# Kernel optimization log

Measured on AMD Instinct MI355X. Metric: run time of the kernel, lower is better.

The kernel has to match this reference:

```python
import jax, jax.numpy as jnp
import numpy as np

V = 16384      # total nodes
G = 32         # nodes per graph (512 graphs)
D = 256        # node embedding dim == hidden_size
N = 8          # heads
H = 32         # head size
I = 1024       # intermediate size
LN_EPS = 1e-12


def _layer_norm(x, g, b):
    mu = jnp.mean(x, axis=-1, keepdims=True)
    var = jnp.mean(jnp.square(x - mu), axis=-1, keepdims=True)
    return (x - mu) * jax.lax.rsqrt(var + LN_EPS) * g + b


def setup_inputs() -> dict:
    key = jax.random.key(0)
    ks = jax.random.split(key, 5)
    node_embeddings = jax.random.normal(ks[0], (V, D), jnp.float32)
    # fully-connected pairs within each graph of size G (sorted by source node)
    idx = np.arange(V, dtype=np.int32).reshape(-1, G)          # [num_graphs, G]
    src = np.repeat(idx, G, axis=1).reshape(-1)                # [P]
    dst = np.tile(idx, (1, G)).reshape(-1)                     # [P]
    in_graph_node_pairs = jnp.asarray(np.stack([src, dst], axis=-1))  # [P, 2]
    s = 0.02
    return {
        "node_embeddings": node_embeddings,
        "in_graph_node_pairs": in_graph_node_pairs,
        "W_qkv": jax.random.normal(ks[1], (D, 3 * N * H), jnp.float32) * s,
        "W_o": jax.random.normal(ks[2], (N * H, D), jnp.float32) * s,
        "ln1_g": jnp.ones((D,), jnp.float32),
        "ln1_b": jnp.zeros((D,), jnp.float32),
        "W_i": jax.random.normal(ks[3], (D, I), jnp.float32) * s,
        "W_out2": jax.random.normal(ks[4], (I, D), jnp.float32) * s,
        "ln2_g": jnp.ones((D,), jnp.float32),
        "ln2_b": jnp.zeros((D,), jnp.float32),
    }


def reference(node_embeddings, in_graph_node_pairs, W_qkv, W_o, ln1_g, ln1_b,
              W_i, W_out2, ln2_g, ln2_b):
    nV = node_embeddings.shape[0]
    src = in_graph_node_pairs[:, 0]
    dst = in_graph_node_pairs[:, 1]
    # QKV projection -> [V, N, 3H] -> split
    qkv = (node_embeddings @ W_qkv).reshape(nV, N, 3 * H)
    q, k, v = jnp.split(qkv, 3, axis=-1)                       # each [V, N, H]
    # per-pair scores [P, N]
    scores = jnp.einsum('phi,phi->ph', q[src], k[dst]) / jnp.sqrt(jnp.float32(H))
    # segment softmax over source node, all heads at once
    m = jax.ops.segment_max(scores, src, num_segments=nV)       # [V, N]
    e = jnp.exp(scores - m[src])
    denom = jax.ops.segment_sum(e, src, num_segments=nV)        # [V, N]
    w = e / denom[src]                                          # [P, N]
    # weighted value scatter-sum -> [V, N, H]
    wv = w[:, :, None] * v[dst]
    att = jax.ops.segment_sum(wv, src, num_segments=nV).reshape(nV, N * H)
    # output projection + residual + LN
    pre = _layer_norm(att @ W_o + node_embeddings, ln1_g, ln1_b)
    inter = jax.nn.gelu(pre @ W_i, approximate=False)
    out = _layer_norm(inter @ W_out2 + pre, ln2_g, ln2_b)
    return out
```

## Files before the change

### kernel.cpp

```cpp
#include <hip/hip_runtime.h>
#include <math.h>

#define V 16384
#define D 256
#define NH 256
#define THREE_NH 768
#define IDIM 1024
#define LN_EPS 1e-12f
#define SCL 0.17677669529663687f

typedef short s16x8 __attribute__((ext_vector_type(8)));
typedef float f32x4 __attribute__((ext_vector_type(4)));

__device__ inline unsigned short f2bf(float f) {
    unsigned u = __float_as_uint(f);
    u += 0x7fffu + ((u >> 16) & 1u);
    return (unsigned short)(u >> 16);
}
__device__ inline float bf2f(unsigned short s) {
    return __uint_as_float(((unsigned)s) << 16);
}

__device__ inline float fast_erf(float x) {
    float ax = fabsf(x);
    float t  = 1.f / fmaf(0.3275911f, ax, 1.f);
    float p  = fmaf(fmaf(fmaf(fmaf(1.061405429f, t, -1.453152027f), t,
                              1.421413741f), t, -0.284496736f), t, 0.254829592f);
    float e  = 1.f - p * t * __expf(-ax * ax);
    return copysignf(e, x);
}

__device__ inline void gl2lds16(const unsigned short* g, unsigned short* l) {
    __builtin_amdgcn_global_load_lds(
        (__attribute__((address_space(1))) void*)(g),
        (__attribute__((address_space(3))) void*)(l), 16, 0, 0);
}

template <int ROWS_T>
__device__ inline void stage(const unsigned short* __restrict__ src, size_t row0,
                             int ldk, int k0, unsigned short* lds, int wv, int lane) {
    constexpr int PER_WAVE = ROWS_T / 32;
    #pragma unroll
    for (int i = 0; i < PER_WAVE; ++i) {
        const int seg = wv * PER_WAVE + i;
        const int r = seg * 8 + (lane >> 3);
        const int c = (lane & 7) ^ (r & 7);
        gl2lds16(src + (row0 + (size_t)r) * ldk + k0 + c * 8, lds + seg * 512);
    }
}

__device__ inline s16x8 fragld(const unsigned short* lds, int row, int chunk) {
    return *(const s16x8*)&lds[row * 64 + ((chunk ^ (row & 7)) << 3)];
}

__global__ __launch_bounds__(256) void prep(const float* __restrict__ X,
                                            unsigned short* __restrict__ Xb,
                                            const float* __restrict__ Wqkv,
                                            const float* __restrict__ Wo,
                                            const float* __restrict__ Wi,
                                            const float* __restrict__ Wo2,
                                            unsigned short* __restrict__ WqkvT,
                                            unsigned short* __restrict__ WoT,
                                            unsigned short* __restrict__ WiT,
                                            unsigned short* __restrict__ Wo2T) {
    const int b = blockIdx.x, t = threadIdx.x;
    if (b >= 768) {
        int i = (b - 768) * 256 + t;
        float4 v = ((const float4*)X)[i];
        ushort4 o;
        o.x = f2bf(v.x); o.y = f2bf(v.y); o.z = f2bf(v.z); o.w = f2bf(v.w);
        ((ushort4*)Xb)[i] = o;
        return;
    }
    __shared__ float tile[32][33];
    const float* W; unsigned short* Wt; int K, N, bx, by;
    if (b < 192)      { W = Wqkv; Wt = WqkvT; K = 256;  N = 768;  bx = b & 7;          by = b >> 3; }
    else if (b < 256) { W = Wo;   Wt = WoT;   K = 256;  N = 256;  bx = (b - 192) & 7;  by = (b - 192) >> 3; }
    else if (b < 512) { W = Wi;   Wt = WiT;   K = 256;  N = 1024; bx = (b - 256) & 7;  by = (b - 256) >> 3; }
    else              { W = Wo2;  Wt = Wo2T;  K = 1024; N = 256;  bx = (b - 512) & 31; by = (b - 512) >> 5; }
    const int k0 = bx * 32, n0 = by * 32;
    #pragma unroll
    for (int p = 0; p < 4; ++p) {
        int idx = t + p * 256, r = idx >> 5, c = idx & 31;
        tile[r][c] = W[(size_t)(k0 + r) * N + n0 + c];
    }
    __syncthreads();
    #pragma unroll
    for (int p = 0; p < 4; ++p) {
        int idx = t + p * 256, r = idx >> 5, c = idx & 31;
        Wt[(size_t)(n0 + r) * K + k0 + c] = f2bf(tile[c][r]);
    }
}

template <int K, int N, int EPI>
__global__ __launch_bounds__(256) void gemm128(const unsigned short* __restrict__ A,
                                               const unsigned short* __restrict__ Bt,
                                               unsigned short* __restrict__ C) {
    __shared__ unsigned short As[128 * 64];
    __shared__ unsigned short Bs[128 * 64];
    constexpr int NCOL = N / 128;
    const int b = blockIdx.x;
    const int idx = b >> 3;
    const int r0 = ((b & 7) * 16 + idx / NCOL) * 128;
    const int c0 = (idx % NCOL) * 128;
    const int t = threadIdx.x;
    const int wv = t >> 6, lane = t & 63, q = lane >> 4, l16 = lane & 15;
    const int wr = (wv >> 1) * 64, wc = (wv & 1) * 64;
    f32x4 acc[4][4] = {};

    for (int k0 = 0; k0 < K; k0 += 64) {
        __syncthreads();
        stage<128>(A,  (size_t)r0, K, k0, As, wv, lane);
        stage<128>(Bt, (size_t)c0, K, k0, Bs, wv, lane);
        __builtin_amdgcn_s_waitcnt(0);
        __syncthreads();
        #pragma unroll
        for (int kk2 = 0; kk2 < 2; ++kk2) {
            s16x8 af[4], bfr[4];
            #pragma unroll
            for (int mf = 0; mf < 4; ++mf)
                af[mf] = fragld(As, wr + mf * 16 + l16, kk2 * 4 + q);
            #pragma unroll
            for (int nf = 0; nf < 4; ++nf)
                bfr[nf] = fragld(Bs, wc + nf * 16 + l16, kk2 * 4 + q);
            #pragma unroll
            for (int mf = 0; mf < 4; ++mf)
                #pragma unroll
                for (int nf = 0; nf < 4; ++nf)
                    acc[mf][nf] = __builtin_amdgcn_mfma_f32_16x16x32_bf16(af[mf], bfr[nf], acc[mf][nf], 0, 0, 0);
        }
    }

    #pragma unroll
    for (int mf = 0; mf < 4; ++mf)
        #pragma unroll
        for (int nf = 0; nf < 4; ++nf) {
            const int cg = c0 + wc + nf * 16 + l16;
            #pragma unroll
            for (int r = 0; r < 4; ++r) {
                const int rg = r0 + wr + mf * 16 + q * 4 + r;
                float v = acc[mf][nf][r];
                if (EPI == 1) v = 0.5f * v * (1.f + fast_erf(v * 0.70710678118654752f));
                C[(size_t)rg * N + cg] = f2bf(v);
            }
        }
}

template <int K, bool OUTF, bool RESBF>
__global__ __launch_bounds__(256) void gemm_ln(const unsigned short* __restrict__ A,
                                               const unsigned short* __restrict__ Bt,
                                               const void* __restrict__ resv,
                                               const float* __restrict__ gamma,
                                               const float* __restrict__ beta,
                                               float* __restrict__ outf,
                                               unsigned short* __restrict__ outb) {
    __shared__ unsigned short As[2][32 * 64];
    __shared__ unsigned short Bs[2][256 * 64];
    __shared__ float2 partial[4][32];
    __shared__ float2 stats[32];
    const int t = threadIdx.x, r0 = blockIdx.x * 32;
    const int wv = t >> 6, lane = t & 63, q = lane >> 4, l16 = lane & 15;
    const int wc = wv * 64;
    f32x4 acc[2][4] = {};

    for (int k0 = 0; k0 < K; k0 += 128) {
        __syncthreads();
        stage<32>(A, (size_t)r0, K, k0,      As[0], wv, lane);
        stage<32>(A, (size_t)r0, K, k0 + 64, As[1], wv, lane);
        stage<256>(Bt, 0, K, k0,      Bs[0], wv, lane);
        stage<256>(Bt, 0, K, k0 + 64, Bs[1], wv, lane);
        __builtin_amdgcn_s_waitcnt(0);
        __syncthreads();
        #pragma unroll
        for (int sub = 0; sub < 2; ++sub) {
            #pragma unroll
            for (int kk2 = 0; kk2 < 2; ++kk2) {
                s16x8 af[2], bfr[4];
                #pragma unroll
                for (int mf = 0; mf < 2; ++mf)
                    af[mf] = fragld(As[sub], mf * 16 + l16, kk2 * 4 + q);
                #pragma unroll
                for (int nf = 0; nf < 4; ++nf)
                    bfr[nf] = fragld(Bs[sub], wc + nf * 16 + l16, kk2 * 4 + q);
                #pragma unroll
                for (int mf = 0; mf < 2; ++mf)
                    #pragma unroll
                    for (int nf = 0; nf < 4; ++nf)
                        acc[mf][nf] = __builtin_amdgcn_mfma_f32_16x16x32_bf16(af[mf], bfr[nf], acc[mf][nf], 0, 0, 0);
            }
        }
    }

    #pragma unroll
    for (int mf = 0; mf < 2; ++mf)
        #pragma unroll
        for (int nf = 0; nf < 4; ++nf) {
            const int cg = wc + nf * 16 + l16;
            #pragma unroll
            for (int r = 0; r < 4; ++r) {
                const size_t idx = (size_t)(r0 + mf * 16 + q * 4 + r) * NH + cg;
                float rv;
                if (RESBF) rv = bf2f(((const unsigned short*)resv)[idx]);
                else       rv = ((const float*)resv)[idx];
                acc[mf][nf][r] += rv;
            }
        }

    #pragma unroll
    for (int mf = 0; mf < 2; ++mf) {
        float s[4] = {0.f, 0.f, 0.f, 0.f}, ss[4] = {0.f, 0.f, 0.f, 0.f};
        #pragma unroll
        for (int nf = 0; nf < 4; ++nf)
            #pragma unroll
            for (int r = 0; r < 4; ++r) {
                float v = acc[mf][nf][r];
                s[r] += v; ss[r] += v * v;
            }
        #pragma unroll
        for (int off = 1; off < 16; off <<= 1)
            #pragma unroll
            for (int r = 0; r < 4; ++r) {
                s[r]  += __shfl_xor(s[r],  off);
                ss[r] += __shfl_xor(ss[r], off);
            }
        if (l16 == 0)
            #pragma unroll
            for (int r = 0; r < 4; ++r)
                partial[wv][mf * 16 + q * 4 + r] = make_float2(s[r], ss[r]);
    }
    __syncthreads();
    if (t < 32) {
        float s = 0.f, ss = 0.f;
        #pragma unroll
        for (int w = 0; w < 4; ++w) { s += partial[w][t].x; ss += partial[w][t].y; }
        float mu  = s * (1.f / 256.f);
        float var = ss * (1.f / 256.f) - mu * mu;
        stats[t] = make_float2(mu, rsqrtf(var + LN_EPS));
    }
    __syncthreads();

    #pragma unroll
    for (int mf = 0; mf < 2; ++mf)
        #pragma unroll
        for (int nf = 0; nf < 4; ++nf) {
            const int cg = wc + nf * 16 + l16;
            const float g = gamma[cg], b = beta[cg];
            #pragma unroll
            for (int r = 0; r < 4; ++r) {
                const int rl = mf * 16 + q * 4 + r;
                const float2 st = stats[rl];
                float v = (acc[mf][nf][r] - st.x) * st.y * g + b;
                const size_t idx = (size_t)(r0 + rl) * NH + cg;
                if (OUTF) outf[idx] = v;
                else      outb[idx] = f2bf(v);
            }
        }
}

__global__ __launch_bounds__(256) void attln(const unsigned short* __restrict__ qkv,
                                             const unsigned short* __restrict__ WoT,
                                             const float* __restrict__ X,
                                             const float* __restrict__ gamma,
                                             const float* __restrict__ beta,
                                             unsigned short* __restrict__ preb) {
    __shared__ unsigned short smem[25216];
    unsigned short* Ks = smem;
    unsigned short* Vt = smem + 8192;
    unsigned short* Ps = smem + 16384;
    unsigned short* at = smem;
    unsigned short* Bs = smem + 8192;
    float2* partial = (float2*)(smem + 24576);
    float2* stats   = (float2*)(smem + 24576 + 512);

    const int g = blockIdx.x, t = threadIdx.x;
    const int wv = t >> 6, lane = t & 63, q = lane >> 4, l16 = lane & 15;
    const unsigned short* src = qkv + (size_t)g * 32 * THREE_NH;

    s16x8 qf[2][2];
    #pragma unroll
    for (int hh = 0; hh < 2; ++hh)
        #pragma unroll
        for (int mf = 0; mf < 2; ++mf)
            qf[hh][mf] = *(const s16x8*)&src[(size_t)(mf * 16 + l16) * THREE_NH +
                                             (wv * 2 + hh) * 96 + q * 8];

    s16x8 vld[4];
    int vh[4], vj[4], vdc[4];
    #pragma unroll
    for (int i = 0; i < 4; ++i) {
        int cid = i * 256 + t;
        vh[i] = cid >> 7; int rem = cid & 127; vj[i] = rem >> 2; vdc[i] = rem & 3;
        vld[i] = *(const s16x8*)&src[(size_t)vj[i] * THREE_NH + vh[i] * 96 + 64 + vdc[i] * 8];
    }

    #pragma unroll
    for (int i = 0; i < 4; ++i) {
        int ck = (wv * 4 + i) * 64 + lane;
        int h = ck >> 7, j = (ck >> 2) & 31, c = ck & 3;
        gl2lds16(src + (size_t)j * THREE_NH + h * 96 + 32 + c * 8, Ks + (wv * 4 + i) * 512);
    }

    #pragma unroll
    for (int i = 0; i < 4; ++i)
        #pragma unroll
        for (int e = 0; e < 8; ++e) {
            int d = vdc[i] * 8 + e;
            Vt[vh[i] * 1024 + d * 32 + ((((vj[i] >> 3) ^ ((d >> 2) & 3))) << 3) + (vj[i] & 7)] =
                (unsigned short)vld[i][e];
        }

    __builtin_amdgcn_s_waitcnt(0);
    __syncthreads();

    f32x4 sacc[2][2][2] = {};
    #pragma unroll
    for (int hh = 0; hh < 2; ++hh) {
        const int h = wv * 2 + hh;
        #pragma unroll
        for (int nf = 0; nf < 2; ++nf) {
            s16x8 kf = *(const s16x8*)&Ks[h * 1024 + (nf * 16 + l16) * 32 + q * 8];
            #pragma unroll
            for (int mf = 0; mf < 2; ++mf)
                sacc[hh][mf][nf] = __builtin_amdgcn_mfma_f32_16x16x32_bf16(
                    qf[hh][mf], kf, sacc[hh][mf][nf], 0, 0, 0);
        }
    }

    float inv[2][2][4];
    #pragma unroll
    for (int hh = 0; hh < 2; ++hh) {
        const int h = wv * 2 + hh;
        #pragma unroll
        for (int mf = 0; mf < 2; ++mf)
            #pragma unroll
            for (int r = 0; r < 4; ++r) {
                float a0 = sacc[hh][mf][0][r], a1 = sacc[hh][mf][1][r];
                float m = fmaxf(a0, a1);
                m = fmaxf(m, __shfl_xor(m, 1));
                m = fmaxf(m, __shfl_xor(m, 2));
                m = fmaxf(m, __shfl_xor(m, 4));
                m = fmaxf(m, __shfl_xor(m, 8));
                float e0 = __expf((a0 - m) * SCL);
                float e1 = __expf((a1 - m) * SCL);
                float sm = e0 + e1;
                sm += __shfl_xor(sm, 1);
                sm += __shfl_xor(sm, 2);
                sm += __shfl_xor(sm, 4);
                sm += __shfl_xor(sm, 8);
                inv[hh][mf][r] = 1.f / sm;
                const int row = mf * 16 + q * 4 + r;
                const int base = h * 1024 + row * 32 + (l16 & 7);
                Ps[base + ((((l16 >> 3) ^ q)) << 3)]       = f2bf(e0);
                Ps[base + ((((2 + (l16 >> 3)) ^ q)) << 3)] = f2bf(e1);
            }
    }

    f32x4 oacc[2][2][2] = {};
    #pragma unroll
    for (int hh = 0; hh < 2; ++hh) {
        const int h = wv * 2 + hh;
        const int sw = (l16 >> 2) & 3;
        s16x8 pa[2], vb[2];
        #pragma unroll
        for (int mf = 0; mf < 2; ++mf)
            pa[mf] = *(const s16x8*)&Ps[h * 1024 + (mf * 16 + l16) * 32 + ((q ^ sw) << 3)];
        #pragma unroll
        for (int nf = 0; nf < 2; ++nf)
            vb[nf] = *(const s16x8*)&Vt[h * 1024 + (nf * 16 + l16) * 32 + ((q ^ sw) << 3)];
        #pragma unroll
        for (int mf = 0; mf < 2; ++mf)
            #pragma unroll
            for (int nf = 0; nf < 2; ++nf)
                oacc[hh][mf][nf] = __builtin_amdgcn_mfma_f32_16x16x32_bf16(
                    pa[mf], vb[nf], oacc[hh][mf][nf], 0, 0, 0);
    }
    __syncthreads();

    #pragma unroll
    for (int hh = 0; hh < 2; ++hh)
        #pragma unroll
        for (int mf = 0; mf < 2; ++mf)
            #pragma unroll
            for (int nf = 0; nf < 2; ++nf)
                #pragma unroll
                for (int r = 0; r < 4; ++r) {
                    float val = oacc[hh][mf][nf][r] * inv[hh][mf][r];
                    const int i = mf * 16 + q * 4 + r;
                    const int col = (wv * 2 + hh) * 32 + nf * 16 + l16;
                    const int kb = col >> 6, c = (col >> 3) & 7;
                    at[kb * 2048 + i * 64 + ((c ^ (i & 7)) << 3) + (col & 7)] = f2bf(val);
                }

    const int wc = wv * 64;
    const int r0 = g * 32;
    f32x4 acc[2][4] = {};

    for (int k0 = 0; k0 < 256; k0 += 64) {
        __syncthreads();
        stage<256>(WoT, 0, 256, k0, Bs, wv, lane);
        __builtin_amdgcn_s_waitcnt(0);
        __syncthreads();
        const unsigned short* atk = at + (k0 >> 6) * 2048;
        #pragma unroll
        for (int kk2 = 0; kk2 < 2; ++kk2) {
            s16x8 af[2], bfr[4];
            #pragma unroll
            for (int mf = 0; mf < 2; ++mf)
                af[mf] = fragld(atk, mf * 16 + l16, kk2 * 4 + q);
            #pragma unroll
            for (int nf = 0; nf < 4; ++nf)
                bfr[nf] = fragld(Bs, wc + nf * 16 + l16, kk2 * 4 + q);
            #pragma unroll
            for (int mf = 0; mf < 2; ++mf)
                #pragma unroll
                for (int nf = 0; nf < 4; ++nf)
                    acc[mf][nf] = __builtin_amdgcn_mfma_f32_16x16x32_bf16(af[mf], bfr[nf], acc[mf][nf], 0, 0, 0);
        }
    }

    #pragma unroll
    for (int mf = 0; mf < 2; ++mf)
        #pragma unroll
        for (int nf = 0; nf < 4; ++nf) {
            const int cg = wc + nf * 16 + l16;
            #pragma unroll
            for (int r = 0; r < 4; ++r)
                acc[mf][nf][r] += X[(size_t)(r0 + mf * 16 + q * 4 + r) * NH + cg];
        }

    #pragma unroll
    for (int mf = 0; mf < 2; ++mf) {
        float sp[4] = {0.f, 0.f, 0.f, 0.f}, ssp[4] = {0.f, 0.f, 0.f, 0.f};
        #pragma unroll
        for (int nf = 0; nf < 4; ++nf)
            #pragma unroll
            for (int r = 0; r < 4; ++r) {
                float v = acc[mf][nf][r];
                sp[r] += v; ssp[r] += v * v;
            }
        #pragma unroll
        for (int off = 1; off < 16; off <<= 1)
            #pragma unroll
            for (int r = 0; r < 4; ++r) {
                sp[r]  += __shfl_xor(sp[r],  off);
                ssp[r] += __shfl_xor(ssp[r], off);
            }
        if (l16 == 0)
            #pragma unroll
            for (int r = 0; r < 4; ++r)
                partial[wv * 32 + mf * 16 + q * 4 + r] = make_float2(sp[r], ssp[r]);
    }
    __syncthreads();
    if (t < 32) {
        float sv = 0.f, ssv = 0.f;
        #pragma unroll
        for (int w = 0; w < 4; ++w) { sv += partial[w * 32 + t].x; ssv += partial[w * 32 + t].y; }
        float mu  = sv * (1.f / 256.f);
        float var = ssv * (1.f / 256.f) - mu * mu;
        stats[t] = make_float2(mu, rsqrtf(var + LN_EPS));
    }
    __syncthreads();

    #pragma unroll
    for (int mf = 0; mf < 2; ++mf)
        #pragma unroll
        for (int nf = 0; nf < 4; ++nf) {
            const int cg = wc + nf * 16 + l16;
            const float gm = gamma[cg], bt = beta[cg];
            #pragma unroll
            for (int r = 0; r < 4; ++r) {
                const int rl = mf * 16 + q * 4 + r;
                const float2 st = stats[rl];
                float v = (acc[mf][nf][r] - st.x) * st.y * gm + bt;
                preb[(size_t)(r0 + rl) * NH + cg] = f2bf(v);
            }
        }
}

extern "C" void kernel_launch(void* const* d_in, const int* in_sizes, int n_in,
                              void* d_out, int out_size, void* d_ws, size_t ws_size,
                              hipStream_t stream) {
    const float* X      = (const float*)d_in[0];
    const float* W_qkv  = (const float*)d_in[2];
    const float* W_o    = (const float*)d_in[3];
    const float* ln1_g  = (const float*)d_in[4];
    const float* ln1_b  = (const float*)d_in[5];
    const float* W_i    = (const float*)d_in[6];
    const float* W_out2 = (const float*)d_in[7];
    const float* ln2_g  = (const float*)d_in[8];
    const float* ln2_b  = (const float*)d_in[9];
    float* out = (float*)d_out;

    char* ws = (char*)d_ws;
    unsigned short* Xbf   = (unsigned short*)(ws);
    unsigned short* qkvb  = (unsigned short*)(ws + 8388608);
    unsigned short* preb  = (unsigned short*)(ws + 58720256);
    unsigned short* WqkvT = (unsigned short*)(ws + 67108864);
    unsigned short* WoT   = (unsigned short*)(ws + 67502080);
    unsigned short* WiT   = (unsigned short*)(ws + 67633152);
    unsigned short* Wo2T  = (unsigned short*)(ws + 68157440);
    unsigned short* interb = (unsigned short*)(ws);

    dim3 blk(256);
    hipLaunchKernelGGL(prep, dim3(768 + V * D / 4 / 256), blk, 0, stream,
                       X, Xbf, W_qkv, W_o, W_i, W_out2, WqkvT, WoT, WiT, Wo2T);

    hipLaunchKernelGGL((gemm128<D, THREE_NH, 0>), dim3(V / 128 * (THREE_NH / 128)), blk, 0, stream,
                       Xbf, WqkvT, qkvb);
    hipLaunchKernelGGL(attln, dim3(V / 32), blk, 0, stream,
                       qkvb, WoT, X, ln1_g, ln1_b, preb);
    hipLaunchKernelGGL((gemm128<D, IDIM, 1>), dim3(V / 128 * (IDIM / 128)), blk, 0, stream,
                       preb, WiT, interb);
    hipLaunchKernelGGL((gemm_ln<IDIM, true, true>), dim3(V / 32), blk, 0, stream,
                       interb, Wo2T, (const void*)preb, ln2_g, ln2_b, out, (unsigned short*)nullptr);
}
```

Before: 160.3 us.

## Fuse FFN up-projection, GELU and down-projection with LayerNorm into one kernel

Replaces the separate GELU up-projection GEMM and the down-projection+LN GEMM with a single per-32-row kernel. It keeps the pre-LN row block in LDS and computes each 256-wide chunk of the intermediate activation into a swizzled LDS buffer, then consumes it immediately. This removes the write and re-read of the 32 MB bf16 intermediate tensor and one launch. In exchange it loses the 128x128 tiling of the up-projection, uses single-buffered weight staging with a sync per 64-wide k step, and needs more LDS per block, which limits occupancy.

```diff
diff --git a/kernel.cpp b/kernel.cpp
--- a/kernel.cpp
+++ b/kernel.cpp
@@ -146,47 +146,85 @@
         }
 }
 
-template <int K, bool OUTF, bool RESBF>
-__global__ __launch_bounds__(256) void gemm_ln(const unsigned short* __restrict__ A,
-                                               const unsigned short* __restrict__ Bt,
-                                               const void* __restrict__ resv,
-                                               const float* __restrict__ gamma,
-                                               const float* __restrict__ beta,
-                                               float* __restrict__ outf,
-                                               unsigned short* __restrict__ outb) {
-    __shared__ unsigned short As[2][32 * 64];
-    __shared__ unsigned short Bs[2][256 * 64];
+__global__ __launch_bounds__(256) void ffn_ln(const unsigned short* __restrict__ preb,
+                                              const unsigned short* __restrict__ WiT,
+                                              const unsigned short* __restrict__ Wo2T,
+                                              const float* __restrict__ gamma,
+                                              const float* __restrict__ beta,
+                                              float* __restrict__ out) {
+    __shared__ unsigned short Apre[32 * 64 * 4];
+    __shared__ unsigned short Bs[256 * 64];
+    __shared__ unsigned short Pbuf[32 * 64 * 4];
     __shared__ float2 partial[4][32];
     __shared__ float2 stats[32];
     const int t = threadIdx.x, r0 = blockIdx.x * 32;
     const int wv = t >> 6, lane = t & 63, q = lane >> 4, l16 = lane & 15;
     const int wc = wv * 64;
-    f32x4 acc[2][4] = {};
-
-    for (int k0 = 0; k0 < K; k0 += 128) {
-        __syncthreads();
-        stage<32>(A, (size_t)r0, K, k0,      As[0], wv, lane);
-        stage<32>(A, (size_t)r0, K, k0 + 64, As[1], wv, lane);
-        stage<256>(Bt, 0, K, k0,      Bs[0], wv, lane);
-        stage<256>(Bt, 0, K, k0 + 64, Bs[1], wv, lane);
-        __builtin_amdgcn_s_waitcnt(0);
-        __syncthreads();
-        #pragma unroll
-        for (int sub = 0; sub < 2; ++sub) {
+    f32x4 acc2[2][4] = {};
+
+    #pragma unroll
+    for (int kc = 0; kc < 4; ++kc)
+        stage<32>(preb, (size_t)r0, 256, kc * 64, Apre + kc * 2048, wv, lane);
+
+    for (int nc = 0; nc < 4; ++nc) {
+        f32x4 acc1[2][4] = {};
+        for (int k0 = 0; k0 < 256; k0 += 64) {
+            __syncthreads();
+            stage<256>(WiT, (size_t)nc * 256, 256, k0, Bs, wv, lane);
+            __builtin_amdgcn_s_waitcnt(0);
+            __syncthreads();
+            const unsigned short* Ak = Apre + (k0 >> 6) * 2048;
             #pragma unroll
             for (int kk2 = 0; kk2 < 2; ++kk2) {
                 s16x8 af[2], bfr[4];
                 #pragma unroll
                 for (int mf = 0; mf < 2; ++mf)
-                    af[mf] = fragld(As[sub], mf * 16 + l16, kk2 * 4 + q);
+                    af[mf] = fragld(Ak, mf * 16 + l16, kk2 * 4 + q);
                 #pragma unroll
                 for (int nf = 0; nf < 4; ++nf)
-                    bfr[nf] = fragld(Bs[sub], wc + nf * 16 + l16, kk2 * 4 + q);
+                    bfr[nf] = fragld(Bs, wc + nf * 16 + l16, kk2 * 4 + q);
                 #pragma unroll
                 for (int mf = 0; mf < 2; ++mf)
                     #pragma unroll
                     for (int nf = 0; nf < 4; ++nf)
-                        acc[mf][nf] = __builtin_amdgcn_mfma_f32_16x16x32_bf16(af[mf], bfr[nf], acc[mf][nf], 0, 0, 0);
+                        acc1[mf][nf] = __builtin_amdgcn_mfma_f32_16x16x32_bf16(af[mf], bfr[nf], acc1[mf][nf], 0, 0, 0);
+            }
+        }
+
+        #pragma unroll
+        for (int mf = 0; mf < 2; ++mf)
+            #pragma unroll
+            for (int nf = 0; nf < 4; ++nf)
+                #pragma unroll
+                for (int r = 0; r < 4; ++r) {
+                    float v = acc1[mf][nf][r];
+                    v = 0.5f * v * (1.f + fast_erf(v * 0.70710678118654752f));
+                    const int i = mf * 16 + q * 4 + r;
+                    const int colc = wc + nf * 16 + l16;
+                    const int c8 = (colc >> 3) & 7;
+                    Pbuf[wv * 2048 + i * 64 + ((c8 ^ (i & 7)) << 3) + (colc & 7)] = f2bf(v);
+                }
+
+        for (int ks = 0; ks < 256; ks += 64) {
+            __syncthreads();
+            stage<256>(Wo2T, 0, IDIM, nc * 256 + ks, Bs, wv, lane);
+            __builtin_amdgcn_s_waitcnt(0);
+            __syncthreads();
+            const unsigned short* Pk = Pbuf + (ks >> 6) * 2048;
+            #pragma unroll
+            for (int kk2 = 0; kk2 < 2; ++kk2) {
+                s16x8 af[2], bfr[4];
+                #pragma unroll
+                for (int mf = 0; mf < 2; ++mf)
+                    af[mf] = fragld(Pk, mf * 16 + l16, kk2 * 4 + q);
+                #pragma unroll
+                for (int nf = 0; nf < 4; ++nf)
+                    bfr[nf] = fragld(Bs, wc + nf * 16 + l16, kk2 * 4 + q);
+                #pragma unroll
+                for (int mf = 0; mf < 2; ++mf)
+                    #pragma unroll
+                    for (int nf = 0; nf < 4; ++nf)
+                        acc2[mf][nf] = __builtin_amdgcn_mfma_f32_16x16x32_bf16(af[mf], bfr[nf], acc2[mf][nf], 0, 0, 0);
             }
         }
     }
@@ -196,13 +234,11 @@
         #pragma unroll
         for (int nf = 0; nf < 4; ++nf) {
             const int cg = wc + nf * 16 + l16;
-            #pragma unroll
-            for (int r = 0; r < 4; ++r) {
-                const size_t idx = (size_t)(r0 + mf * 16 + q * 4 + r) * NH + cg;
-                float rv;
-                if (RESBF) rv = bf2f(((const unsigned short*)resv)[idx]);
-                else       rv = ((const float*)resv)[idx];
-                acc[mf][nf][r] += rv;
+            const int kb = cg >> 6, c8 = (cg >> 3) & 7, e = cg & 7;
+            #pragma unroll
+            for (int r = 0; r < 4; ++r) {
+                const int i = mf * 16 + q * 4 + r;
+                acc2[mf][nf][r] += bf2f(Apre[kb * 2048 + i * 64 + ((c8 ^ (i & 7)) << 3) + e]);
             }
         }
 
@@ -213,7 +249,7 @@
         for (int nf = 0; nf < 4; ++nf)
             #pragma unroll
             for (int r = 0; r < 4; ++r) {
-                float v = acc[mf][nf][r];
+                float v = acc2[mf][nf][r];
                 s[r] += v; ss[r] += v * v;
             }
         #pragma unroll
@@ -249,10 +285,7 @@
             for (int r = 0; r < 4; ++r) {
                 const int rl = mf * 16 + q * 4 + r;
                 const float2 st = stats[rl];
-                float v = (acc[mf][nf][r] - st.x) * st.y * g + b;
-                const size_t idx = (size_t)(r0 + rl) * NH + cg;
-                if (OUTF) outf[idx] = v;
-                else      outb[idx] = f2bf(v);
+                out[(size_t)(r0 + rl) * NH + cg] = (acc2[mf][nf][r] - st.x) * st.y * g + b;
             }
         }
 }
@@ -499,7 +532,6 @@
     unsigned short* WoT   = (unsigned short*)(ws + 67502080);
     unsigned short* WiT   = (unsigned short*)(ws + 67633152);
     unsigned short* Wo2T  = (unsigned short*)(ws + 68157440);
-    unsigned short* interb = (unsigned short*)(ws);
 
     dim3 blk(256);
     hipLaunchKernelGGL(prep, dim3(768 + V * D / 4 / 256), blk, 0, stream,
@@ -509,8 +541,6 @@
                        Xbf, WqkvT, qkvb);
     hipLaunchKernelGGL(attln, dim3(V / 32), blk, 0, stream,
                        qkvb, WoT, X, ln1_g, ln1_b, preb);
-    hipLaunchKernelGGL((gemm128<D, IDIM, 1>), dim3(V / 128 * (IDIM / 128)), blk, 0, stream,
-                       preb, WiT, interb);
-    hipLaunchKernelGGL((gemm_ln<IDIM, true, true>), dim3(V / 32), blk, 0, stream,
-                       interb, Wo2T, (const void*)preb, ln2_g, ln2_b, out, (unsigned short*)nullptr);
-}
+    hipLaunchKernelGGL(ffn_ln, dim3(V / 32), blk, 0, stream,
+                       preb, WiT, Wo2T, ln2_g, ln2_b, out);
+}
```

Measured after the change: 158.1 us. No clear change (-1.4%).
